# Kernel tuning notes

Hardware: AMD Instinct MI355X
Metric: run time of the kernel (lower is better)

Reference implementation:

```python
import jax, jax.numpy as jnp
import numpy as np

N_OBJ, N_REL = 2048, 32768
OBJ_DIM, POOL, H, E, C = 4096, 2048, 512, 200, 151
GEO = 128
IMG_W, IMG_H = 1024.0, 768.0
NUM_ITER = 3


def _lin(x, W, b):
    return x @ W.T + b


def _gru(x, h, Wih, Whh, bih, bhh):
    # torch.nn.GRUCell math; gates stacked (r, z, n)
    gi = x @ Wih.T + bih
    gh = h @ Whh.T + bhh
    i_r, i_z, i_n = jnp.split(gi, 3, axis=-1)
    h_r, h_z, h_n = jnp.split(gh, 3, axis=-1)
    r = jax.nn.sigmoid(i_r + h_r)
    z = jax.nn.sigmoid(i_z + h_z)
    n = jnp.tanh(i_n + r * h_n)
    return (1.0 - z) * n + z * h


def _box_info(boxes, norm=None):
    # [x1,y1,x2,y2,cx,cy,w,h]
    wh = boxes[:, 2:4] - boxes[:, 0:2] + 1.0
    ctr = boxes[:, 0:2] + 0.5 * wh
    info = jnp.concatenate([boxes, ctr, wh], axis=1)
    return info / norm if norm is not None else info


def _box_pair_info(b1, b2):
    # b1,b2: [R,8] normalized box infos -> [R,32]
    ub = jnp.stack([jnp.minimum(b1[:, 0], b2[:, 0]), jnp.minimum(b1[:, 1], b2[:, 1]),
                    jnp.maximum(b1[:, 2], b2[:, 2]), jnp.maximum(b1[:, 3], b2[:, 3])], axis=1)
    ib = jnp.stack([jnp.maximum(b1[:, 0], b2[:, 0]), jnp.maximum(b1[:, 1], b2[:, 1]),
                    jnp.minimum(b1[:, 2], b2[:, 2]), jnp.minimum(b1[:, 3], b2[:, 3])], axis=1)
    inter = _box_info(ib)
    bad = (ib[:, 2] < ib[:, 0]) | (ib[:, 3] < ib[:, 1])
    inter = jnp.where(bad[:, None], 0.0, inter)
    return jnp.concatenate([b1, b2, _box_info(ub), inter], axis=1)


def _encode_box_info(boxes):
    # motifs 9-d geometry encoding
    wh = boxes[:, 2:4] - boxes[:, 0:2] + 1.0
    xy = boxes[:, 0:2] + 0.5 * wh
    w, h = wh[:, 0:1], wh[:, 1:2]
    x, y = xy[:, 0:1], xy[:, 1:2]
    x1, y1, x2, y2 = boxes[:, 0:1], boxes[:, 1:2], boxes[:, 2:3], boxes[:, 3:4]
    return jnp.concatenate([w / IMG_W, h / IMG_H, x / IMG_W, y / IMG_H, x1 / IMG_W,
                            y1 / IMG_H, x2 / IMG_W, y2 / IMG_H, w * h / (IMG_W * IMG_H)], axis=1)


def _forward(inst_roi_feats, union_features, boxes, emb_dist_W, emb_label_W, up_W, up_b,
             pairup_W, pairup_b, pos1_W, pos1_b, bn_g, bn_b, bn_m, bn_v, pos2_W, pos2_b,
             spt1_W, spt1_b, spt2_W, spt2_b, pairfin_W, pairfin_b, objhid_W, objhid_b,
             objfin_W, objfin_b, objU_W, objU_b, edgeU_W, edgeU_b,
             egru_Wih, egru_Whh, egru_bih, egru_bhh, ngru_Wih, ngru_Whh, ngru_bih, ngru_bhh,
             svw_W, svw_b, ovw_W, ovw_b, obj_labels, sub_idx, obj_idx):
    # ---- PairwiseFeatureExtractor ----
    # pos_embed: fc(9,32) -> eval BatchNorm1d(32) -> fc(32,128) -> ReLU
    p = _lin(_encode_box_info(boxes), pos1_W, pos1_b)
    p = (p - bn_m) * bn_g / jnp.sqrt(bn_v + 1e-5) + bn_b
    pos_embed = jax.nn.relu(_lin(p, pos2_W, pos2_b))
    emb_dist = emb_dist_W[obj_labels]                       # predcls: embed GT labels
    aug = _lin(jnp.concatenate([inst_roi_feats, emb_dist, pos_embed], 1), objhid_W, objhid_b)
    augment = jnp.concatenate([emb_label_W[obj_labels], inst_roi_feats, aug], 1)  # [N,4808]
    # pairwise (edge) features: gather head/tail reps + spatial gating
    obox = _box_info(boxes, norm=max(IMG_W, IMG_H, 100.0))  # [N,8]
    fused = _lin(augment, pairup_W, pairup_b).reshape(-1, 2, H)
    pair = jnp.concatenate([fused[:, 0][sub_idx], fused[:, 1][obj_idx]], 1)  # [R,1024]
    geo = _box_pair_info(obox[sub_idx], obox[obj_idx])      # [R,32]
    spt = jax.nn.relu(_lin(jax.nn.relu(_lin(geo, spt1_W, spt1_b)), spt2_W, spt2_b))
    rel_feats = jax.nn.relu(_lin(pair * spt, pairfin_W, pairfin_b))
    rel_feats = rel_feats + _lin(union_features, up_W, up_b)  # 'fusion' + dim-up
    obj_feats = jax.nn.relu(_lin(augment, objfin_W, objfin_b))
    # ---- IMP iterative message passing ----
    obj_rep = _lin(obj_feats, objU_W, objU_b)
    rel_rep = jax.nn.relu(_lin(rel_feats, edgeU_W, edgeU_b))
    vert = _gru(obj_rep, jnp.zeros_like(obj_rep), ngru_Wih, ngru_Whh, ngru_bih, ngru_bhh)
    edge = _gru(rel_rep, jnp.zeros_like(rel_rep), egru_Wih, egru_Whh, egru_bih, egru_bhh)
    n = vert.shape[0]
    for _ in range(NUM_ITER):
        sv, ov = vert[sub_idx], vert[obj_idx]
        ws = jax.nn.sigmoid(_lin(jnp.concatenate([sv, edge], 1), svw_W, svw_b))  # [R,1]
        wo = jax.nn.sigmoid(_lin(jnp.concatenate([ov, edge], 1), ovw_W, ovw_b))
        new_edge = _gru(ws * sv + wo * ov, edge, egru_Wih, egru_Whh, egru_bih, egru_bhh)
        # sub2rel @ (ws*edge) + obj2rel @ (wo*edge) == segment sums over pair indices
        ctx = jax.ops.segment_sum(ws * edge, sub_idx, n) + jax.ops.segment_sum(wo * edge, obj_idx, n)
        vert = _gru(ctx, vert, ngru_Wih, ngru_Whh, ngru_bih, ngru_bhh)
        edge = new_edge
    return vert, edge


def setup_inputs() -> dict:
    keys = jax.random.split(jax.random.key(0), 64)
    ki = iter(keys)

    def nrm(shape, s=0.02):
        return (jax.random.normal(next(ki), shape) * s).astype(jnp.float32)

    kb = jax.random.split(next(ki), 4)
    x1 = jax.random.uniform(kb[0], (N_OBJ,)) * (IMG_W - 200.0)
    y1 = jax.random.uniform(kb[1], (N_OBJ,)) * (IMG_H - 150.0)
    x2 = x1 + 1.0 + jax.random.uniform(kb[2], (N_OBJ,)) * 199.0
    y2 = y1 + 1.0 + jax.random.uniform(kb[3], (N_OBJ,)) * 149.0
    boxes = jnp.stack([x1, y1, x2, y2], axis=1).astype(jnp.float32)

    inp = {
        'inst_roi_feats': nrm((N_OBJ, OBJ_DIM), 1.0),
        'union_features': nrm((N_REL, OBJ_DIM), 1.0),
        'boxes': boxes,
        'emb_dist_W': nrm((C, E)), 'emb_label_W': nrm((C, E)),
        'up_W': nrm((POOL, OBJ_DIM)), 'up_b': jnp.zeros((POOL,), jnp.float32),
        'pairup_W': nrm((2 * H, H + OBJ_DIM + E)), 'pairup_b': jnp.zeros((2 * H,), jnp.float32),
        'pos1_W': nrm((32, 9)), 'pos1_b': jnp.zeros((32,), jnp.float32),
        'bn_g': jnp.ones((32,), jnp.float32), 'bn_b': jnp.zeros((32,), jnp.float32),
        'bn_m': nrm((32,)), 'bn_v': jnp.ones((32,), jnp.float32),
        'pos2_W': nrm((GEO, 32)), 'pos2_b': jnp.zeros((GEO,), jnp.float32),
        'spt1_W': nrm((H, 32)), 'spt1_b': jnp.zeros((H,), jnp.float32),
        'spt2_W': nrm((2 * H, H)), 'spt2_b': jnp.zeros((2 * H,), jnp.float32),
        'pairfin_W': nrm((POOL, 2 * H)), 'pairfin_b': jnp.zeros((POOL,), jnp.float32),
        'objhid_W': nrm((H, OBJ_DIM + E + GEO)), 'objhid_b': jnp.zeros((H,), jnp.float32),
        'objfin_W': nrm((POOL, H + OBJ_DIM + E)), 'objfin_b': jnp.zeros((POOL,), jnp.float32),
        'objU_W': nrm((H, POOL)), 'objU_b': jnp.zeros((H,), jnp.float32),
        'edgeU_W': nrm((H, POOL)), 'edgeU_b': jnp.zeros((H,), jnp.float32),
        'egru_Wih': nrm((3 * H, H)), 'egru_Whh': nrm((3 * H, H)),
        'egru_bih': jnp.zeros((3 * H,), jnp.float32), 'egru_bhh': jnp.zeros((3 * H,), jnp.float32),
        'ngru_Wih': nrm((3 * H, H)), 'ngru_Whh': nrm((3 * H, H)),
        'ngru_bih': jnp.zeros((3 * H,), jnp.float32), 'ngru_bhh': jnp.zeros((3 * H,), jnp.float32),
        'svw_W': nrm((1, 2 * H)), 'svw_b': jnp.zeros((1,), jnp.float32),
        'ovw_W': nrm((1, 2 * H)), 'ovw_b': jnp.zeros((1,), jnp.float32),
        'obj_labels': jax.random.randint(next(ki), (N_OBJ,), 0, C),
        'sub_idx': jax.random.randint(next(ki), (N_REL,), 0, N_OBJ),
        'obj_idx': jax.random.randint(next(ki), (N_REL,), 0, N_OBJ),
    }
    return inp


def reference(inst_roi_feats, union_features, boxes, emb_dist_W, emb_label_W, up_W, up_b,
              pairup_W, pairup_b, pos1_W, pos1_b, bn_g, bn_b, bn_m, bn_v, pos2_W, pos2_b,
              spt1_W, spt1_b, spt2_W, spt2_b, pairfin_W, pairfin_b, objhid_W, objhid_b,
              objfin_W, objfin_b, objU_W, objU_b, edgeU_W, edgeU_b,
              egru_Wih, egru_Whh, egru_bih, egru_bhh, ngru_Wih, ngru_Whh, ngru_bih, ngru_bhh,
              svw_W, svw_b, ovw_W, ovw_b, obj_labels, sub_idx, obj_idx):
    return _forward(inst_roi_feats, union_features, boxes, emb_dist_W, emb_label_W, up_W, up_b,
                    pairup_W, pairup_b, pos1_W, pos1_b, bn_g, bn_b, bn_m, bn_v, pos2_W, pos2_b,
                    spt1_W, spt1_b, spt2_W, spt2_b, pairfin_W, pairfin_b, objhid_W, objhid_b,
                    objfin_W, objfin_b, objU_W, objU_b, edgeU_W, edgeU_b,
                    egru_Wih, egru_Whh, egru_bih, egru_bhh, ngru_Wih, ngru_Whh, ngru_bih, ngru_bhh,
                    svw_W, svw_b, ovw_W, ovw_b, obj_labels, sub_idx, obj_idx)
```

## Files before the change

kernel.cpp:

```cpp
#include <hip/hip_runtime.h>
#include <stdint.h>

#define NOBJ 2048
#define NREL 32768

typedef __attribute__((ext_vector_type(8))) short short8;
typedef __attribute__((ext_vector_type(4))) float f32x4;
typedef __attribute__((ext_vector_type(4))) unsigned short ushort4v;

__device__ __forceinline__ unsigned short f2bs(float x){
  unsigned u = __float_as_uint(x);
  unsigned v = u + 0x7fffu + ((u >> 16) & 1u);
  return (unsigned short)(v >> 16);
}
__device__ __forceinline__ float b2f(unsigned short u){
  return __uint_as_float(((unsigned)u) << 16);
}
__device__ __forceinline__ float sigf(float x){ return 1.0f / (1.0f + expf(-x)); }

__device__ __forceinline__ void gload16(const unsigned short* g, unsigned short* l) {
  __builtin_amdgcn_global_load_lds(
      (const __attribute__((address_space(1))) unsigned int*)(uintptr_t)g,
      (__attribute__((address_space(3))) unsigned int*)(uintptr_t)l,
      16, 0, 0);
}

template<int RMODE, bool ACCUM, bool OUTB, bool PRODF, bool AF32>
__global__ __launch_bounds__(256, 2)
void gemm_bt(const void* __restrict__ Ap, const unsigned short* __restrict__ B,
             const float* __restrict__ bias, const float* __restrict__ Cin,
             void* __restrict__ Cp, int M, int N, int K, int lda, int ldc,
             const unsigned short* __restrict__ fusedp,
             const int* __restrict__ subp, const int* __restrict__ objp)
{
  __shared__ __align__(16) unsigned short As[128 * 64];
  __shared__ __align__(16) unsigned short Bs[128 * 64];
  const int t = threadIdx.x;
  const int lane = t & 63;
  const int w = t >> 6;
  const int nwg = gridDim.x;
  const int q8 = nwg >> 3, r8 = nwg & 7;
  const int xcd = blockIdx.x & 7, bidx = blockIdx.x >> 3;
  const int wgid = (xcd < r8 ? xcd * (q8 + 1) : r8 * (q8 + 1) + (xcd - r8) * q8) + bidx;
  const int ntile = N >> 7;
  const int bm = wgid / ntile;
  const int bn = wgid - bm * ntile;
  const int m0 = bm << 7, n0 = bn << 7;
  const int wm = (w & 1) << 6, wn = (w >> 1) << 6;
  const int lrow = lane & 15, kg = lane >> 4;
  const int rx = lrow & 7;

  const int srow8 = lane >> 3;
  const int sslot = ((lane & 7) ^ srow8) << 3;
  const unsigned short* Bg = B + (long)(n0 + w * 8 + srow8) * K + sslot;
  const long ldb32 = (long)32 * K;

  const unsigned short* Ag = nullptr;
  const float* afp = nullptr;
  long lda32 = 0;
  int ar0 = 0;
  unsigned short* abase = nullptr;
  if constexpr (AF32) {
    ar0 = t >> 4;
    const int ac4 = t & 15;
    afp = (const float*)Ap + (long)(m0 + ar0) * lda + (ac4 << 2);
    abase = As + ((((ac4 >> 1) ^ (ar0 & 7)) << 3) + ((ac4 & 1) << 2));
  } else {
    Ag = (const unsigned short*)Ap + (long)(m0 + w * 8 + srow8) * lda + sslot;
    lda32 = (long)32 * lda;
  }

  f32x4 acc[4][4] = {};

  for (int k0 = 0; k0 < K; k0 += 64) {
#pragma unroll
    for (int q = 0; q < 4; q++)
      gload16(Bg + q * ldb32 + k0, Bs + (q * 32 + w * 8) * 64);
    if constexpr (AF32) {
      const float* ap = afp + k0;
#pragma unroll
      for (int j = 0; j < 8; j++) {
        f32x4 v = *(const f32x4*)(ap + (long)j * 16 * lda);
        ushort4v o;
        o[0] = f2bs(v[0]); o[1] = f2bs(v[1]); o[2] = f2bs(v[2]); o[3] = f2bs(v[3]);
        *(ushort4v*)(abase + (ar0 + j * 16) * 64) = o;
      }
    } else {
#pragma unroll
      for (int q = 0; q < 4; q++)
        gload16(Ag + q * lda32 + k0, As + (q * 32 + w * 8) * 64);
    }
    __syncthreads();
    short8 afr[4][2], bfr[4][2];
#pragma unroll
    for (int i = 0; i < 4; i++) {
      const int ra = wm + i * 16 + lrow;
#pragma unroll
      for (int ks = 0; ks < 2; ks++)
        afr[i][ks] = *(const short8*)(As + ra * 64 + (((ks * 4 + kg) ^ rx) << 3));
    }
#pragma unroll
    for (int j = 0; j < 4; j++) {
      const int rb = wn + j * 16 + lrow;
#pragma unroll
      for (int ks = 0; ks < 2; ks++)
        bfr[j][ks] = *(const short8*)(Bs + rb * 64 + (((ks * 4 + kg) ^ rx) << 3));
    }
#pragma unroll
    for (int i = 0; i < 4; i++)
#pragma unroll
      for (int j = 0; j < 4; j++)
#pragma unroll
        for (int ks = 0; ks < 2; ks++)
          acc[i][j] = __builtin_amdgcn_mfma_f32_16x16x32_bf16(afr[i][ks], bfr[j][ks], acc[i][j], 0, 0, 0);
    __syncthreads();
  }

  float* Cf = (float*)Cp;
  unsigned short* Cb = (unsigned short*)Cp;
#pragma unroll
  for (int i = 0; i < 4; i++) {
#pragma unroll
    for (int j = 0; j < 4; j++) {
      const int col = n0 + wn + j * 16 + lrow;
      const float bv = bias[col];
#pragma unroll
      for (int q = 0; q < 4; q++) {
        const long row = m0 + wm + i * 16 + kg * 4 + q;
        float v = acc[i][j][q] + bv;
        if constexpr (RMODE == 1) v = fmaxf(v, 0.0f);
        if constexpr (PRODF) {
          int gr = (col < 512) ? subp[row] : objp[row];
          v *= b2f(fusedp[(long)gr * 1024 + col]);
        }
        if constexpr (ACCUM) v += Cin[row * (long)N + col];
        if constexpr (RMODE == 2) v = fmaxf(v, 0.0f);
        if constexpr (OUTB) Cb[row * (long)ldc + col] = f2bs(v);
        else Cf[row * (long)ldc + col] = v;
      }
    }
  }
}


__global__ void cvt_pad4(const float* __restrict__ src, unsigned short* __restrict__ dst,
                         int rows, int K0, int Kp)
{
  const int kp4 = Kp >> 2;
  const long total = (long)rows * kp4;
  for (long i = blockIdx.x * (long)blockDim.x + threadIdx.x; i < total; i += (long)gridDim.x * blockDim.x) {
    int r = (int)(i / kp4), k = (int)(i - (long)r * kp4) << 2;
    ushort4v o;
    if (k < K0) {
      f32x4 v = *(const f32x4*)(src + (long)r * K0 + k);
      o[0] = f2bs(v[0]); o[1] = f2bs(v[1]); o[2] = f2bs(v[2]); o[3] = f2bs(v[3]);
    } else {
      o[0] = 0; o[1] = 0; o[2] = 0; o[3] = 0;
    }
    *(ushort4v*)(dst + (long)r * Kp + k) = o;
  }
}

__global__ void cvt4(const float* __restrict__ src, unsigned short* __restrict__ dst, long n4)
{
  for (long i = blockIdx.x * (long)blockDim.x + threadIdx.x; i < n4; i += (long)gridDim.x * blockDim.x) {
    f32x4 v = ((const f32x4*)src)[i];
    ushort4v o;
    o[0] = f2bs(v[0]); o[1] = f2bs(v[1]); o[2] = f2bs(v[2]); o[3] = f2bs(v[3]);
    ((ushort4v*)dst)[i] = o;
  }
}

__global__ void transpose_cvt(const float* __restrict__ src, unsigned short* __restrict__ dst,
                              int R, int C)
{
  __shared__ float tile[32][33];
  int c0 = blockIdx.x * 32, r0 = blockIdx.y * 32;
  for (int i = threadIdx.y; i < 32; i += 8)
    tile[i][threadIdx.x] = src[(long)(r0 + i) * C + c0 + threadIdx.x];
  __syncthreads();
  for (int i = threadIdx.y; i < 32; i += 8)
    dst[(long)(c0 + i) * R + r0 + threadIdx.x] = f2bs(tile[threadIdx.x][i]);
}

__global__ void comp_bias(const float* __restrict__ edgeU_W, const float* __restrict__ up_b,
                          const float* __restrict__ edgeU_b, float* __restrict__ b_comp)
{
  int j = (int)((blockIdx.x * (long)blockDim.x + threadIdx.x) >> 6);
  int l = threadIdx.x & 63;
  if (j >= 512) return;
  float s = 0.0f;
  for (int k = l; k < 2048; k += 64) s += edgeU_W[(long)j * 2048 + k] * up_b[k];
#pragma unroll
  for (int off = 32; off > 0; off >>= 1) s += __shfl_xor(s, off);
  if (l == 0) b_comp[j] = s + edgeU_b[j];
}

__global__ void bias_cat(const float* __restrict__ bhh, float* __restrict__ out)
{
  int j = blockIdx.x * blockDim.x + threadIdx.x;
  if (j < 3072) out[j] = (j < 1536) ? 0.0f : bhh[j - 1536];
}

__global__ void obox_k(const float* __restrict__ boxes, float* __restrict__ obox)
{
  int i = blockIdx.x * blockDim.x + threadIdx.x;
  if (i >= NOBJ) return;
  float x1 = boxes[i*4], y1 = boxes[i*4+1], x2 = boxes[i*4+2], y2 = boxes[i*4+3];
  float wdt = x2 - x1 + 1.0f, hgt = y2 - y1 + 1.0f;
  float cx = x1 + 0.5f * wdt, cy = y1 + 0.5f * hgt;
  const float inv = 1.0f / 1024.0f;
  float* o = obox + i * 8;
  o[0]=x1*inv; o[1]=y1*inv; o[2]=x2*inv; o[3]=y2*inv;
  o[4]=cx*inv; o[5]=cy*inv; o[6]=wdt*inv; o[7]=hgt*inv;
}

__global__ void posembed_k(const float* __restrict__ boxes,
                           const float* __restrict__ w1, const float* __restrict__ b1,
                           const float* __restrict__ g, const float* __restrict__ bb,
                           const float* __restrict__ mm, const float* __restrict__ vv,
                           const float* __restrict__ w2, const float* __restrict__ b2,
                           float* __restrict__ out)
{
  int o = blockIdx.x, t = threadIdx.x;
  __shared__ float e[9];
  __shared__ float p[32];
  if (t == 0) {
    float x1 = boxes[o*4], y1 = boxes[o*4+1], x2 = boxes[o*4+2], y2 = boxes[o*4+3];
    float wdt = x2 - x1 + 1.0f, hgt = y2 - y1 + 1.0f;
    float cx = x1 + 0.5f * wdt, cy = y1 + 0.5f * hgt;
    e[0]=wdt/1024.0f; e[1]=hgt/768.0f; e[2]=cx/1024.0f; e[3]=cy/768.0f;
    e[4]=x1/1024.0f;  e[5]=y1/768.0f;  e[6]=x2/1024.0f; e[7]=y2/768.0f;
    e[8]=wdt*hgt/(1024.0f*768.0f);
  }
  __syncthreads();
  if (t < 32) {
    float s = b1[t];
#pragma unroll
    for (int j = 0; j < 9; j++) s += w1[t*9+j] * e[j];
    s = (s - mm[t]) * g[t] / sqrtf(vv[t] + 1e-5f) + bb[t];
    p[t] = s;
  }
  __syncthreads();
  float s = b2[t];
#pragma unroll
  for (int j = 0; j < 32; j++) s += w2[t*32+j] * p[j];
  out[o*128 + t] = fmaxf(s, 0.0f);
}

__device__ __forceinline__ void pack8_store(unsigned short* dst, f32x4 a, f32x4 b)
{
  ushort4v o0, o1;
  o0[0]=f2bs(a[0]); o0[1]=f2bs(a[1]); o0[2]=f2bs(a[2]); o0[3]=f2bs(a[3]);
  o1[0]=f2bs(b[0]); o1[1]=f2bs(b[1]); o1[2]=f2bs(b[2]); o1[3]=f2bs(b[3]);
  *(ushort4v*)dst = o0;
  *(ushort4v*)(dst + 4) = o1;
}

__global__ void build_x1(const float* __restrict__ inst, const float* __restrict__ embd,
                         const int* __restrict__ labels, const float* __restrict__ pose,
                         unsigned short* __restrict__ X1b)
{
  const long total = (long)NOBJ * 560;
  for (long i = blockIdx.x * (long)blockDim.x + threadIdx.x; i < total; i += (long)gridDim.x * blockDim.x) {
    int r = (int)(i / 560), c = ((int)(i - (long)r * 560)) << 3;
    unsigned short* dst = X1b + (long)r * 4480 + c;
    const float* src;
    if (c < 4096)      src = inst + (long)r * 4096 + c;
    else if (c < 4296) src = embd + (long)labels[r] * 200 + (c - 4096);
    else if (c < 4424) src = pose + r * 128 + (c - 4296);
    else { ushort4v z = {0,0,0,0}; *(ushort4v*)dst = z; *(ushort4v*)(dst+4) = z; continue; }
    pack8_store(dst, *(const f32x4*)src, *((const f32x4*)src + 1));
  }
}

__global__ void build_aug(const float* __restrict__ embl, const int* __restrict__ labels,
                          const float* __restrict__ inst, unsigned short* __restrict__ augb)
{
  const long total = (long)NOBJ * 608;
  for (long i = blockIdx.x * (long)blockDim.x + threadIdx.x; i < total; i += (long)gridDim.x * blockDim.x) {
    int r = (int)(i / 608), c = ((int)(i - (long)r * 608)) << 3;
    if (c >= 4296 && c < 4808) continue;
    unsigned short* dst = augb + (long)r * 4864 + c;
    const float* src;
    if (c < 200)       src = embl + (long)labels[r] * 200 + c;
    else if (c < 4296) src = inst + (long)r * 4096 + (c - 200);
    else { ushort4v z = {0,0,0,0}; *(ushort4v*)dst = z; *(ushort4v*)(dst+4) = z; continue; }
    pack8_store(dst, *(const f32x4*)src, *((const f32x4*)src + 1));
  }
}

__global__ void build_geo(const float* __restrict__ obox, const int* __restrict__ sub,
                          const int* __restrict__ obj, unsigned short* __restrict__ geob)
{
  int r = blockIdx.x * blockDim.x + threadIdx.x;
  if (r >= NREL) return;
  const float* b1 = obox + sub[r] * 8;
  const float* b2 = obox + obj[r] * 8;
  float o[32];
#pragma unroll
  for (int j = 0; j < 8; j++) { o[j] = b1[j]; o[8+j] = b2[j]; }
  float ux1 = fminf(b1[0], b2[0]), uy1 = fminf(b1[1], b2[1]);
  float ux2 = fmaxf(b1[2], b2[2]), uy2 = fmaxf(b1[3], b2[3]);
  float uw = ux2 - ux1 + 1.0f, uh = uy2 - uy1 + 1.0f;
  o[16]=ux1; o[17]=uy1; o[18]=ux2; o[19]=uy2;
  o[20]=ux1+0.5f*uw; o[21]=uy1+0.5f*uh; o[22]=uw; o[23]=uh;
  float ix1 = fmaxf(b1[0], b2[0]), iy1 = fmaxf(b1[1], b2[1]);
  float ix2 = fminf(b1[2], b2[2]), iy2 = fminf(b1[3], b2[3]);
  bool bad = (ix2 < ix1) || (iy2 < iy1);
  float iw = ix2 - ix1 + 1.0f, ih = iy2 - iy1 + 1.0f;
  if (bad) {
#pragma unroll
    for (int j = 24; j < 32; j++) o[j] = 0.0f;
  } else {
    o[24]=ix1; o[25]=iy1; o[26]=ix2; o[27]=iy2;
    o[28]=ix1+0.5f*iw; o[29]=iy1+0.5f*ih; o[30]=iw; o[31]=ih;
  }
  unsigned short* gp = geob + (long)r * 64;
#pragma unroll
  for (int j = 0; j < 32; j++) gp[j] = f2bs(o[j]);
#pragma unroll
  for (int j = 32; j < 64; j++) gp[j] = 0;
}

__global__ void gru_init_v(const unsigned short* __restrict__ gi, const float* __restrict__ bhh,
                           float* __restrict__ h, unsigned short* __restrict__ hb, int n)
{
  const long total = (long)n * 64;
  for (long i = blockIdx.x * (long)blockDim.x + threadIdx.x; i < total; i += (long)gridDim.x * blockDim.x) {
    int r = (int)(i >> 6), c = ((int)(i & 63)) << 3;
    const unsigned short* gr = gi + (long)r * 1536;
    short8 vr = *(const short8*)(gr + c);
    short8 vz = *(const short8*)(gr + 512 + c);
    short8 vn = *(const short8*)(gr + 1024 + c);
    float hv[8];
#pragma unroll
    for (int k = 0; k < 8; k++) {
      float rr = sigf(b2f((unsigned short)vr[k]) + bhh[c + k]);
      float z  = sigf(b2f((unsigned short)vz[k]) + bhh[512 + c + k]);
      float nn = tanhf(b2f((unsigned short)vn[k]) + rr * bhh[1024 + c + k]);
      hv[k] = (1.0f - z) * nn;
    }
    float* hp = h + (long)r * 512 + c;
    *(f32x4*)hp = *(f32x4*)hv;
    *(f32x4*)(hp + 4) = *(f32x4*)(hv + 4);
    pack8_store(hb + (long)r * 512 + c, *(f32x4*)hv, *(f32x4*)(hv + 4));
  }
}

__global__ void gru_init_e(const unsigned short* __restrict__ gi, const float* __restrict__ bhh,
                           unsigned short* __restrict__ hb, int n)
{
  const long total = (long)n * 64;
  for (long i = blockIdx.x * (long)blockDim.x + threadIdx.x; i < total; i += (long)gridDim.x * blockDim.x) {
    int r = (int)(i >> 6), c = ((int)(i & 63)) << 3;
    const unsigned short* gr = gi + (long)r * 1536;
    short8 vr = *(const short8*)(gr + c);
    short8 vz = *(const short8*)(gr + 512 + c);
    short8 vn = *(const short8*)(gr + 1024 + c);
    float hv[8];
#pragma unroll
    for (int k = 0; k < 8; k++) {
      float rr = sigf(b2f((unsigned short)vr[k]) + bhh[c + k]);
      float z  = sigf(b2f((unsigned short)vz[k]) + bhh[512 + c + k]);
      float nn = tanhf(b2f((unsigned short)vn[k]) + rr * bhh[1024 + c + k]);
      hv[k] = (1.0f - z) * nn;
    }
    pack8_store(hb + (long)r * 512 + c, *(f32x4*)hv, *(f32x4*)(hv + 4));
  }
}

__global__ void gru_step_v(const unsigned short* __restrict__ gi, const unsigned short* __restrict__ gh,
                           int ghs, const float* __restrict__ hin, float* __restrict__ hout,
                           unsigned short* __restrict__ hb, int n)
{
  const long total = (long)n * 64;
  for (long i = blockIdx.x * (long)blockDim.x + threadIdx.x; i < total; i += (long)gridDim.x * blockDim.x) {
    int r = (int)(i >> 6), c = ((int)(i & 63)) << 3;
    const unsigned short* gr = gi + (long)r * 1536;
    const unsigned short* hr = gh + (long)r * ghs;
    short8 ir = *(const short8*)(gr + c);
    short8 iz = *(const short8*)(gr + 512 + c);
    short8 in_ = *(const short8*)(gr + 1024 + c);
    short8 hrr = *(const short8*)(hr + c);
    short8 hz = *(const short8*)(hr + 512 + c);
    short8 hn = *(const short8*)(hr + 1024 + c);
    const float* hi = hin + (long)r * 512 + c;
    f32x4 h0 = *(const f32x4*)hi;
    f32x4 h1 = *(const f32x4*)(hi + 4);
    float hv[8];
#pragma unroll
    for (int k = 0; k < 8; k++) {
      float rr = sigf(b2f((unsigned short)ir[k]) + b2f((unsigned short)hrr[k]));
      float z  = sigf(b2f((unsigned short)iz[k]) + b2f((unsigned short)hz[k]));
      float nn = tanhf(b2f((unsigned short)in_[k]) + rr * b2f((unsigned short)hn[k]));
      float old = (k < 4) ? h0[k] : h1[k - 4];
      hv[k] = (1.0f - z) * nn + z * old;
    }
    float* hp = hout + (long)r * 512 + c;
    *(f32x4*)hp = *(f32x4*)hv;
    *(f32x4*)(hp + 4) = *(f32x4*)(hv + 4);
    pack8_store(hb + (long)r * 512 + c, *(f32x4*)hv, *(f32x4*)(hv + 4));
  }
}

__global__ __launch_bounds__(256)
void gru_step_e2(const unsigned short* __restrict__ GH, const unsigned short* __restrict__ VG,
                 const float* __restrict__ ws_arr_in, const float* __restrict__ wo_arr_in,
                 float* __restrict__ ws_arr_out, float* __restrict__ wo_arr_out,
                 const int* __restrict__ sub, const int* __restrict__ obj,
                 const float* __restrict__ bih,
                 unsigned short* __restrict__ edgeb, float* __restrict__ fout,
                 const unsigned short* __restrict__ vertb,
                 const float* __restrict__ svwW, const float* __restrict__ svwb,
                 const float* __restrict__ ovwW, const float* __restrict__ ovwb,
                 int compute_w, int n)
{
  long gid = blockIdx.x * 256L + threadIdx.x;
  int r = (int)(gid >> 6);
  int l = (int)(gid & 63);
  if (r >= n) return;
  const int c = l << 3;
  int s = sub[r], o = obj[r];
  float ws = ws_arr_in[r], wo = wo_arr_in[r];
  const unsigned short* gh = GH + (long)r * 1536;
  const unsigned short* vs = VG + (long)s * 3072;
  const unsigned short* vo = VG + (long)o * 3072;
  short8 ghr = *(const short8*)(gh + c);
  short8 ghz = *(const short8*)(gh + 512 + c);
  short8 ghn = *(const short8*)(gh + 1024 + c);
  short8 vsr = *(const short8*)(vs + c);
  short8 vsz = *(const short8*)(vs + 512 + c);
  short8 vsn = *(const short8*)(vs + 1024 + c);
  short8 vor_ = *(const short8*)(vo + c);
  short8 voz = *(const short8*)(vo + 512 + c);
  short8 von = *(const short8*)(vo + 1024 + c);
  short8 hold = *(const short8*)(edgeb + (long)r * 512 + c);
  float hv[8];
#pragma unroll
  for (int k = 0; k < 8; k++) {
    float gir = ws * b2f((unsigned short)vsr[k]) + wo * b2f((unsigned short)vor_[k]) + bih[c + k];
    float giz = ws * b2f((unsigned short)vsz[k]) + wo * b2f((unsigned short)voz[k]) + bih[512 + c + k];
    float gin = ws * b2f((unsigned short)vsn[k]) + wo * b2f((unsigned short)von[k]) + bih[1024 + c + k];
    float rr = sigf(gir + b2f((unsigned short)ghr[k]));
    float z  = sigf(giz + b2f((unsigned short)ghz[k]));
    float nn = tanhf(gin + rr * b2f((unsigned short)ghn[k]));
    hv[k] = (1.0f - z) * nn + z * b2f((unsigned short)hold[k]);
  }
  pack8_store(edgeb + (long)r * 512 + c, *(f32x4*)hv, *(f32x4*)(hv + 4));
  if (fout) {
    float* fp = fout + (long)r * 512 + c;
    *(f32x4*)fp = *(f32x4*)hv;
    *(f32x4*)(fp + 4) = *(f32x4*)(hv + 4);
  }
  if (compute_w) {
    short8 svv = *(const short8*)(vertb + (long)s * 512 + c);
    short8 ovv = *(const short8*)(vertb + (long)o * 512 + c);
    float as = 0.0f, ao = 0.0f;
#pragma unroll
    for (int k = 0; k < 8; k++) {
      float e = hv[k];
      as += svwW[c + k] * b2f((unsigned short)svv[k]) + svwW[512 + c + k] * e;
      ao += ovwW[c + k] * b2f((unsigned short)ovv[k]) + ovwW[512 + c + k] * e;
    }
#pragma unroll
    for (int off = 32; off > 0; off >>= 1) {
      as += __shfl_xor(as, off);
      ao += __shfl_xor(ao, off);
    }
    if (l == 0) {
      ws_arr_out[r] = sigf(as + svwb[0]);
      wo_arr_out[r] = sigf(ao + ovwb[0]);
    }
  }
}

__global__ __launch_bounds__(256)
void edge_weights(const unsigned short* __restrict__ vertb, const unsigned short* __restrict__ edgeb,
                  const int* __restrict__ sub, const int* __restrict__ obj,
                  const float* __restrict__ svwW, const float* __restrict__ svwb,
                  const float* __restrict__ ovwW, const float* __restrict__ ovwb,
                  float* __restrict__ ws_arr, float* __restrict__ wo_arr)
{
  long gid = blockIdx.x * 256L + threadIdx.x;
  int r = (int)(gid >> 6);
  int l = (int)(gid & 63);
  if (r >= NREL) return;
  int s = sub[r], o = obj[r];
  const unsigned short* sv = vertb + (long)s * 512;
  const unsigned short* ov = vertb + (long)o * 512;
  const unsigned short* e  = edgeb + (long)r * 512;
  float as = 0.0f, ao = 0.0f;
#pragma unroll
  for (int k = 0; k < 8; k++) {
    int c = l + k * 64;
    float svv = b2f(sv[c]), ovv = b2f(ov[c]), ev = b2f(e[c]);
    as += svwW[c] * svv + svwW[512 + c] * ev;
    ao += ovwW[c] * ovv + ovwW[512 + c] * ev;
  }
#pragma unroll
  for (int off = 32; off > 0; off >>= 1) {
    as += __shfl_xor(as, off);
    ao += __shfl_xor(ao, off);
  }
  if (l == 0) {
    ws_arr[r] = sigf(as + svwb[0]);
    wo_arr[r] = sigf(ao + ovwb[0]);
  }
}


__global__ void csr_count(const int* __restrict__ sub, const int* __restrict__ obj,
                          int* __restrict__ cnt)
{
  int r = blockIdx.x * blockDim.x + threadIdx.x;
  if (r >= NREL) return;
  atomicAdd(&cnt[sub[r]], 1);
  atomicAdd(&cnt[obj[r]], 1);
}

__global__ __launch_bounds__(1024)
void csr_scan(const int* __restrict__ cnt, int* __restrict__ off)
{
  __shared__ int a[1024], b[1024];
  int t = threadIdx.x;
  int c0 = cnt[2*t], c1 = cnt[2*t+1];
  a[t] = c0 + c1;
  __syncthreads();
  int* src = a; int* dst = b;
  for (int s = 1; s < 1024; s <<= 1) {
    int v = src[t];
    if (t >= s) v += src[t - s];
    dst[t] = v;
    __syncthreads();
    int* tmp = src; src = dst; dst = tmp;
  }
  int incl = src[t];
  int excl = incl - (c0 + c1);
  off[2*t] = excl;
  off[2*t+1] = excl + c0;
  if (t == 1023) off[2048] = incl;
}

__global__ void csr_fill(const int* __restrict__ sub, const int* __restrict__ obj,
                         const int* __restrict__ off, int* __restrict__ rcur,
                         int* __restrict__ lists)
{
  int r = blockIdx.x * blockDim.x + threadIdx.x;
  if (r >= NREL) return;
  int s = sub[r];
  int p = atomicAdd(&rcur[s], 1);
  lists[off[s] + p] = (r << 1);
  int o = obj[r];
  int q = atomicAdd(&rcur[o], 1);
  lists[off[o] + q] = (r << 1) | 1;
}

__global__ __launch_bounds__(128)
void ctx_gather(const unsigned short* __restrict__ edgeb, const float* __restrict__ ws,
                const float* __restrict__ wo, const int* __restrict__ off,
                const int* __restrict__ lists, unsigned short* __restrict__ ctxb)
{
  __shared__ float part[512];
  int o = blockIdx.x;
  int l = threadIdx.x & 63;
  int w = threadIdx.x >> 6;
  int i0 = off[o], i1 = off[o + 1];
  float acc[8] = {0.f,0.f,0.f,0.f,0.f,0.f,0.f,0.f};
  for (int i = i0 + w; i < i1; i += 2) {
    int e = lists[i];
    int r = e >> 1;
    float sc = (e & 1) ? wo[r] : ws[r];
    short8 row = *(const short8*)(edgeb + (long)r * 512 + l * 8);
#pragma unroll
    for (int k = 0; k < 8; k++) acc[k] += sc * b2f((unsigned short)row[k]);
  }
  if (w == 1) {
    *(f32x4*)&part[l*8]     = *(f32x4*)&acc[0];
    *(f32x4*)&part[l*8 + 4] = *(f32x4*)&acc[4];
  }
  __syncthreads();
  if (w == 0) {
#pragma unroll
    for (int k = 0; k < 8; k++) acc[k] += part[l*8 + k];
    pack8_store(ctxb + (long)o * 512 + l * 8, *(f32x4*)&acc[0], *(f32x4*)&acc[4]);
  }
}


static inline int nblk(long total) {
  long b = (total + 255) / 256;
  return (int)(b > 16384 ? 16384 : b);
}

#define GEMM(RM, AC, OB, PF, grid, Aa, Bb, bb, Ci, Cc, Mm, Nn, Kk, ldA, ldC, fp, sp, op) \
  gemm_bt<RM, AC, OB, PF, false><<<grid, 256, 0, stream>>>(Aa, Bb, bb, Ci, Cc, Mm, Nn, Kk, ldA, ldC, fp, sp, op)
#define GEMMF(RM, AC, OB, grid, Aa, Bb, bb, Ci, Cc, Mm, Nn, Kk, ldA, ldC) \
  gemm_bt<RM, AC, OB, false, true><<<grid, 256, 0, stream>>>(Aa, Bb, bb, Ci, Cc, Mm, Nn, Kk, ldA, ldC, nullptr, nullptr, nullptr)

extern "C" void kernel_launch(void* const* d_in, const int* in_sizes, int n_in,
                              void* d_out, int out_size, void* d_ws, size_t ws_size,
                              hipStream_t stream)
{
  const float* inst     = (const float*)d_in[0];
  const float* unionf   = (const float*)d_in[1];
  const float* boxes    = (const float*)d_in[2];
  const float* embd_W   = (const float*)d_in[3];
  const float* embl_W   = (const float*)d_in[4];
  const float* up_W     = (const float*)d_in[5];
  const float* up_b     = (const float*)d_in[6];
  const float* pairup_W = (const float*)d_in[7];
  const float* pairup_b = (const float*)d_in[8];
  const float* pos1_W   = (const float*)d_in[9];
  const float* pos1_b   = (const float*)d_in[10];
  const float* bn_g     = (const float*)d_in[11];
  const float* bn_b     = (const float*)d_in[12];
  const float* bn_m     = (const float*)d_in[13];
  const float* bn_v     = (const float*)d_in[14];
  const float* pos2_W   = (const float*)d_in[15];
  const float* pos2_b   = (const float*)d_in[16];
  const float* spt1_W   = (const float*)d_in[17];
  const float* spt1_b   = (const float*)d_in[18];
  const float* spt2_W   = (const float*)d_in[19];
  const float* spt2_b   = (const float*)d_in[20];
  const float* pairfin_W= (const float*)d_in[21];
  const float* pairfin_b= (const float*)d_in[22];
  const float* objhid_W = (const float*)d_in[23];
  const float* objhid_b = (const float*)d_in[24];
  const float* objfin_W = (const float*)d_in[25];
  const float* objfin_b = (const float*)d_in[26];
  const float* objU_W   = (const float*)d_in[27];
  const float* objU_b   = (const float*)d_in[28];
  const float* edgeU_W  = (const float*)d_in[29];
  const float* edgeU_b  = (const float*)d_in[30];
  const float* egru_Wih = (const float*)d_in[31];
  const float* egru_Whh = (const float*)d_in[32];
  const float* egru_bih = (const float*)d_in[33];
  const float* egru_bhh = (const float*)d_in[34];
  const float* ngru_Wih = (const float*)d_in[35];
  const float* ngru_Whh = (const float*)d_in[36];
  const float* ngru_bih = (const float*)d_in[37];
  const float* ngru_bhh = (const float*)d_in[38];
  const float* svw_W    = (const float*)d_in[39];
  const float* svw_b    = (const float*)d_in[40];
  const float* ovw_W    = (const float*)d_in[41];
  const float* ovw_b    = (const float*)d_in[42];
  const int*   labels   = (const int*)d_in[43];
  const int*   sub      = (const int*)d_in[44];
  const int*   obj      = (const int*)d_in[45];
  (void)in_sizes; (void)n_in; (void)out_size; (void)ws_size;

  char* base = (char*)d_ws;
  size_t off = 0;
  auto alloc = [&](size_t bytes) -> void* {
    void* p = base + off;
    off += (bytes + 255) & ~(size_t)255;
    return p;
  };

  unsigned short* objhid_Wb  = (unsigned short*)alloc(512L  * 4480 * 2);
  unsigned short* pairup_Wb  = (unsigned short*)alloc(1024L * 4864 * 2);
  unsigned short* objfin_Wb  = (unsigned short*)alloc(2048L * 4864 * 2);
  unsigned short* up_Wtb     = (unsigned short*)alloc(4096L * 2048 * 2);
  unsigned short* pairfin_Wb = (unsigned short*)alloc(2048L * 1024 * 2);
  unsigned short* spt1_Wb    = (unsigned short*)alloc(512L  * 64   * 2);
  unsigned short* spt2_Wb    = (unsigned short*)alloc(1024L * 512  * 2);
  unsigned short* objU_Wb    = (unsigned short*)alloc(512L  * 2048 * 2);
  unsigned short* edgeU_Wb   = (unsigned short*)alloc(512L  * 2048 * 2);
  unsigned short* egru_Wihb  = (unsigned short*)alloc(1536L * 512  * 2);
  unsigned short* egru_Whhb  = (unsigned short*)alloc(1536L * 512  * 2);
  unsigned short* ngru_Wihb  = (unsigned short*)alloc(1536L * 512  * 2);
  unsigned short* vg_Wb      = (unsigned short*)alloc(3072L * 512  * 2);
  unsigned short* W_compb    = (unsigned short*)alloc(512L  * 4096 * 2);
  float*          b_comp     = (float*)alloc(512L * 4);
  float*          zbias      = (float*)alloc(4096L * 4);
  float*          vgbias     = (float*)alloc(3072L * 4);

  float*          obox      = (float*)alloc(NOBJ * 8L * 4);
  float*          pose      = (float*)alloc(NOBJ * 128L * 4);
  unsigned short* obj_featsb= (unsigned short*)alloc((long)NOBJ * 2048 * 2);
  unsigned short* obj_repb  = (unsigned short*)alloc((long)NOBJ * 512 * 2);
  unsigned short* giv       = (unsigned short*)alloc((long)NOBJ * 1536 * 2);
  unsigned short* VGb       = (unsigned short*)alloc((long)NOBJ * 3072 * 2);
  float*          vert      = (float*)alloc((long)NOBJ * 512 * 4);
  unsigned short* vertb     = (unsigned short*)alloc((long)NOBJ * 512 * 2);
  unsigned short* ctxb      = (unsigned short*)alloc((long)NOBJ * 512 * 2);
  unsigned short* geob      = (unsigned short*)alloc((long)NREL * 64 * 2);
  unsigned short* edgeb     = (unsigned short*)alloc((long)NREL * 512 * 2);
  float*          ws_arr    = (float*)alloc((long)NREL * 4);
  float*          wo_arr    = (float*)alloc((long)NREL * 4);

  int* cnt   = (int*)alloc(NOBJ * 4);
  int* coff  = (int*)alloc((NOBJ + 1) * 4);
  int* rcur  = (int*)alloc(NOBJ * 4);
  int* lists = (int*)alloc(2L * NREL * 4);

  char* regA = (char*)alloc((long)NREL * 512 * 4);
  unsigned short* X1b = (unsigned short*)regA;
  float*          T1  = (float*)regA;
  char* regB = (char*)alloc((long)NOBJ * 4864 * 2 > (long)NREL * 512 * 2
                            ? (long)NOBJ * 4864 * 2 : (long)NREL * 512 * 2);
  unsigned short* augb     = (unsigned short*)regB;
  unsigned short* rel_repb = (unsigned short*)regB;
  unsigned short* fusedb = (unsigned short*)alloc((long)NOBJ * 1024 * 2);
  unsigned short* spt1b  = (unsigned short*)alloc((long)NREL * 512 * 2);
  char* big1 = (char*)alloc((long)NREL * 1536 * 4);
  unsigned short* G1    = (unsigned short*)big1;
  unsigned short* prodb = (unsigned short*)(big1 + (long)NREL * 1024 * 4);
  unsigned short* gi_e  = (unsigned short*)big1;
  unsigned short* GHb   = (unsigned short*)big1;

  float* d_out_vert = (float*)d_out;
  float* d_out_edge = (float*)d_out + (long)NOBJ * 512;

  cvt_pad4<<<nblk(512L*4480/4),  256, 0, stream>>>(objhid_W,  objhid_Wb,  512,  4424, 4480);
  cvt_pad4<<<nblk(1024L*4864/4), 256, 0, stream>>>(pairup_W,  pairup_Wb,  1024, 4808, 4864);
  cvt_pad4<<<nblk(2048L*4864/4), 256, 0, stream>>>(objfin_W,  objfin_Wb,  2048, 4808, 4864);
  cvt_pad4<<<nblk(512L*64/4),    256, 0, stream>>>(spt1_W,    spt1_Wb,    512,  32,   64);
  cvt4<<<nblk(2048L*1024/4), 256, 0, stream>>>(pairfin_W, pairfin_Wb, 2048L*1024/4);
  cvt4<<<nblk(1024L*512/4),  256, 0, stream>>>(spt2_W,    spt2_Wb,    1024L*512/4);
  cvt4<<<nblk(512L*2048/4),  256, 0, stream>>>(objU_W,    objU_Wb,    512L*2048/4);
  cvt4<<<nblk(512L*2048/4),  256, 0, stream>>>(edgeU_W,   edgeU_Wb,   512L*2048/4);
  cvt4<<<nblk(1536L*512/4),  256, 0, stream>>>(egru_Wih,  egru_Wihb,  1536L*512/4);
  cvt4<<<nblk(1536L*512/4),  256, 0, stream>>>(egru_Whh,  egru_Whhb,  1536L*512/4);
  cvt4<<<nblk(1536L*512/4),  256, 0, stream>>>(ngru_Wih,  ngru_Wihb,  1536L*512/4);
  cvt4<<<nblk(1536L*512/4),  256, 0, stream>>>(egru_Wih,  vg_Wb,               1536L*512/4);
  cvt4<<<nblk(1536L*512/4),  256, 0, stream>>>(ngru_Whh,  vg_Wb + 1536L*512,   1536L*512/4);
  bias_cat<<<12, 256, 0, stream>>>(ngru_bhh, vgbias);
  transpose_cvt<<<dim3(4096/32, 2048/32), dim3(32, 8), 0, stream>>>(up_W, up_Wtb, 2048, 4096);
  hipMemsetAsync(zbias, 0, 4096L * 4, stream);
  comp_bias<<<128, 256, 0, stream>>>(edgeU_W, up_b, edgeU_b, b_comp);
  GEMM(0,false,true,false, dim3((512>>7)*(4096>>7)), edgeU_Wb, up_Wtb, zbias, nullptr, W_compb, 512, 4096, 2048, 2048, 4096, nullptr, nullptr, nullptr);

  hipMemsetAsync(cnt, 0, NOBJ * 4, stream);
  hipMemsetAsync(rcur, 0, NOBJ * 4, stream);
  csr_count<<<NREL/256, 256, 0, stream>>>(sub, obj, cnt);
  csr_scan<<<1, 1024, 0, stream>>>(cnt, coff);
  csr_fill<<<NREL/256, 256, 0, stream>>>(sub, obj, coff, rcur, lists);

  obox_k<<<(NOBJ + 255) / 256, 256, 0, stream>>>(boxes, obox);
  posembed_k<<<NOBJ, 128, 0, stream>>>(boxes, pos1_W, pos1_b, bn_g, bn_b, bn_m, bn_v,
                                       pos2_W, pos2_b, pose);
  build_x1<<<nblk((long)NOBJ*560), 256, 0, stream>>>(inst, embd_W, labels, pose, X1b);
  build_aug<<<nblk((long)NOBJ*608), 256, 0, stream>>>(embl_W, labels, inst, augb);
  GEMM(0,false,true ,false, dim3((NOBJ>>7)*(512>>7)),  X1b, objhid_Wb, objhid_b, nullptr, augb + 4296, NOBJ, 512, 4480, 4480, 4864, nullptr, nullptr, nullptr);
  GEMM(0,false,true ,false, dim3((NOBJ>>7)*(1024>>7)), augb, pairup_Wb, pairup_b, nullptr, fusedb, NOBJ, 1024, 4864, 4864, 1024, nullptr, nullptr, nullptr);
  GEMM(1,false,true ,false, dim3((NOBJ>>7)*(2048>>7)), augb, objfin_Wb, objfin_b, nullptr, obj_featsb, NOBJ, 2048, 4864, 4864, 2048, nullptr, nullptr, nullptr);
  GEMM(0,false,true ,false, dim3((NOBJ>>7)*(512>>7)),  obj_featsb, objU_Wb, objU_b, nullptr, obj_repb, NOBJ, 512, 2048, 2048, 512, nullptr, nullptr, nullptr);
  GEMM(0,false,true ,false, dim3((NOBJ>>7)*(1536>>7)), obj_repb, ngru_Wihb, ngru_bih, nullptr, giv, NOBJ, 1536, 512, 512, 1536, nullptr, nullptr, nullptr);
  gru_init_v<<<nblk((long)NOBJ*64), 256, 0, stream>>>(giv, ngru_bhh, vert, vertb, NOBJ);

  build_geo<<<(NREL + 255) / 256, 256, 0, stream>>>(obox, sub, obj, geob);
  GEMM(1,false,true ,false, dim3((NREL>>7)*(512>>7)),  geob, spt1_Wb, spt1_b, nullptr, spt1b, NREL, 512, 64, 64, 512, nullptr, nullptr, nullptr);
  GEMM(1,false,true ,true , dim3((NREL>>7)*(1024>>7)), spt1b, spt2_Wb, spt2_b, nullptr, prodb, NREL, 1024, 512, 512, 1024, fusedb, sub, obj);
  GEMM(1,false,true ,false, dim3((NREL>>7)*(2048>>7)), prodb, pairfin_Wb, pairfin_b, nullptr, G1, NREL, 2048, 1024, 1024, 2048, nullptr, nullptr, nullptr);
  GEMMF(0,false,false, dim3((NREL>>7)*(512>>7)), unionf, W_compb, b_comp, nullptr, T1, NREL, 512, 4096, 4096, 512);
  GEMM(2,true ,true ,false, dim3((NREL>>7)*(512>>7)),  G1, edgeU_Wb, zbias, T1, rel_repb, NREL, 512, 2048, 2048, 512, nullptr, nullptr, nullptr);
  GEMM(0,false,true ,false, dim3((NREL>>7)*(1536>>7)), rel_repb, egru_Wihb, egru_bih, nullptr, gi_e, NREL, 1536, 512, 512, 1536, nullptr, nullptr, nullptr);
  gru_init_e<<<nblk((long)NREL*64), 256, 0, stream>>>(gi_e, egru_bhh, edgeb, NREL);

  edge_weights<<<NREL*64/256, 256, 0, stream>>>(vertb, edgeb, sub, obj,
                                                svw_W, svw_b, ovw_W, ovw_b, ws_arr, wo_arr);

  for (int it = 0; it < 3; it++) {
    const bool last = (it == 2);
    ctx_gather<<<NOBJ, 128, 0, stream>>>(edgeb, ws_arr, wo_arr, coff, lists, ctxb);
    GEMM(0,false,true,false, dim3((NOBJ>>7)*(3072>>7)), vertb, vg_Wb, vgbias, nullptr, VGb, NOBJ, 3072, 512, 512, 3072, nullptr, nullptr, nullptr);
    GEMM(0,false,true,false, dim3((NREL>>7)*(1536>>7)), edgeb, egru_Whhb, egru_bhh, nullptr, GHb, NREL, 1536, 512, 512, 1536, nullptr, nullptr, nullptr);
    GEMM(0,false,true,false, dim3((NOBJ>>7)*(1536>>7)), ctxb, ngru_Wihb, ngru_bih, nullptr, giv, NOBJ, 1536, 512, 512, 1536, nullptr, nullptr, nullptr);
    gru_step_v<<<nblk((long)NOBJ*64), 256, 0, stream>>>(giv, VGb + 1536, 3072, vert,
                                                        last ? d_out_vert : vert, vertb, NOBJ);
    gru_step_e2<<<NREL*64/256, 256, 0, stream>>>(GHb, VGb, ws_arr, wo_arr, ws_arr, wo_arr,
                                                 sub, obj, egru_bih, edgeb,
                                                 last ? d_out_edge : nullptr, vertb,
                                                 svw_W, svw_b, ovw_W, ovw_b,
                                                 last ? 0 : 1, NREL);
  }
}
```

Baseline: 1.820 ms.

## Use 64x64-tile GEMM for small-M object GEMMs and batch weight conversions

Adds a 64x64-tile bf16 MFMA GEMM kernel with XCD-aware block remapping and uses it for the object-side GEMMs (M=2048 or 512). These previously launched too few 128x128 tiles to fill the GPU. The nine separate fp32-to-bf16 weight conversion launches are also merged into one multi-segment kernel to save launch overhead. The smaller tiles give more workgroups but less data reuse per tile and a single-buffered K loop.

```diff
diff --git a/kernel.cpp b/kernel.cpp
--- a/kernel.cpp
+++ b/kernel.cpp
@@ -142,6 +142,84 @@
   }
 }
 
+template<int RMODE>
+__global__ __launch_bounds__(256, 2)
+void gemm64(const unsigned short* __restrict__ A, const unsigned short* __restrict__ B,
+            const float* __restrict__ bias, unsigned short* __restrict__ C,
+            int M, int N, int K, int lda, int ldc)
+{
+  __shared__ __align__(16) unsigned short As[64 * 64];
+  __shared__ __align__(16) unsigned short Bs[64 * 64];
+  const int t = threadIdx.x;
+  const int lane = t & 63;
+  const int w = t >> 6;
+  const int nwg = gridDim.x;
+  const int q8 = nwg >> 3, r8 = nwg & 7;
+  const int xcd = blockIdx.x & 7, bidx = blockIdx.x >> 3;
+  const int wgid = (xcd < r8 ? xcd * (q8 + 1) : r8 * (q8 + 1) + (xcd - r8) * q8) + bidx;
+  const int ntile = N >> 6;
+  const int bm = wgid / ntile, bn = wgid - bm * ntile;
+  const int m0 = bm << 6, n0 = bn << 6;
+  const int wm = (w & 1) << 5, wn = (w >> 1) << 5;
+  const int lrow = lane & 15, kg = lane >> 4;
+  const int rx = lrow & 7;
+
+  const int srow8 = lane >> 3;
+  const int sslot = ((lane & 7) ^ srow8) << 3;
+  const unsigned short* Ag = A + (long)(m0 + w * 16 + srow8) * lda + sslot;
+  const unsigned short* Bg = B + (long)(n0 + w * 16 + srow8) * K + sslot;
+  const long lda8 = 8L * lda, ldb8 = 8L * K;
+
+  f32x4 acc[2][2] = {};
+
+  for (int k0 = 0; k0 < K; k0 += 64) {
+    gload16(Ag + k0,        As + (w * 16) * 64);
+    gload16(Ag + lda8 + k0, As + (w * 16 + 8) * 64);
+    gload16(Bg + k0,        Bs + (w * 16) * 64);
+    gload16(Bg + ldb8 + k0, Bs + (w * 16 + 8) * 64);
+    __syncthreads();
+    short8 afr[2][2], bfr[2][2];
+#pragma unroll
+    for (int i = 0; i < 2; i++) {
+      const int ra = wm + i * 16 + lrow;
+#pragma unroll
+      for (int ks = 0; ks < 2; ks++)
+        afr[i][ks] = *(const short8*)(As + ra * 64 + (((ks * 4 + kg) ^ rx) << 3));
+    }
+#pragma unroll
+    for (int j = 0; j < 2; j++) {
+      const int rb = wn + j * 16 + lrow;
+#pragma unroll
+      for (int ks = 0; ks < 2; ks++)
+        bfr[j][ks] = *(const short8*)(Bs + rb * 64 + (((ks * 4 + kg) ^ rx) << 3));
+    }
+#pragma unroll
+    for (int i = 0; i < 2; i++)
+#pragma unroll
+      for (int j = 0; j < 2; j++)
+#pragma unroll
+        for (int ks = 0; ks < 2; ks++)
+          acc[i][j] = __builtin_amdgcn_mfma_f32_16x16x32_bf16(afr[i][ks], bfr[j][ks], acc[i][j], 0, 0, 0);
+    __syncthreads();
+  }
+
+#pragma unroll
+  for (int i = 0; i < 2; i++) {
+#pragma unroll
+    for (int j = 0; j < 2; j++) {
+      const int col = n0 + wn + j * 16 + lrow;
+      const float bv = bias[col];
+#pragma unroll
+      for (int q = 0; q < 4; q++) {
+        const long row = m0 + wm + i * 16 + kg * 4 + q;
+        float v = acc[i][j][q] + bv;
+        if constexpr (RMODE == 1) v = fmaxf(v, 0.0f);
+        C[row * (long)ldc + col] = f2bs(v);
+      }
+    }
+  }
+}
+
 
 __global__ void cvt_pad4(const float* __restrict__ src, unsigned short* __restrict__ dst,
                          int rows, int K0, int Kp)
@@ -161,13 +239,24 @@
   }
 }
 
-__global__ void cvt4(const float* __restrict__ src, unsigned short* __restrict__ dst, long n4)
-{
-  for (long i = blockIdx.x * (long)blockDim.x + threadIdx.x; i < n4; i += (long)gridDim.x * blockDim.x) {
-    f32x4 v = ((const f32x4*)src)[i];
-    ushort4v o;
-    o[0] = f2bs(v[0]); o[1] = f2bs(v[1]); o[2] = f2bs(v[2]); o[3] = f2bs(v[3]);
-    ((ushort4v*)dst)[i] = o;
+struct CvtSeg { const float* src; unsigned short* dst; long base; long n4; };
+struct Cvt9 { CvtSeg s[9]; long total; };
+
+__global__ void cvt4_multi(Cvt9 cfg)
+{
+  for (long i = blockIdx.x * (long)blockDim.x + threadIdx.x; i < cfg.total;
+       i += (long)gridDim.x * blockDim.x) {
+#pragma unroll
+    for (int k = 0; k < 9; k++) {
+      if (i >= cfg.s[k].base && i < cfg.s[k].base + cfg.s[k].n4) {
+        long j = i - cfg.s[k].base;
+        f32x4 v = ((const f32x4*)cfg.s[k].src)[j];
+        ushort4v o;
+        o[0] = f2bs(v[0]); o[1] = f2bs(v[1]); o[2] = f2bs(v[2]); o[3] = f2bs(v[3]);
+        ((ushort4v*)cfg.s[k].dst)[j] = o;
+        break;
+      }
+    }
   }
 }
 
@@ -597,6 +686,8 @@
   gemm_bt<RM, AC, OB, PF, false><<<grid, 256, 0, stream>>>(Aa, Bb, bb, Ci, Cc, Mm, Nn, Kk, ldA, ldC, fp, sp, op)
 #define GEMMF(RM, AC, OB, grid, Aa, Bb, bb, Ci, Cc, Mm, Nn, Kk, ldA, ldC) \
   gemm_bt<RM, AC, OB, false, true><<<grid, 256, 0, stream>>>(Aa, Bb, bb, Ci, Cc, Mm, Nn, Kk, ldA, ldC, nullptr, nullptr, nullptr)
+#define G64(RM, Aa, Bb, bb, Cc, Mm, Nn, Kk, ldA, ldC) \
+  gemm64<RM><<<dim3(((Mm) >> 6) * ((Nn) >> 6)), 256, 0, stream>>>(Aa, Bb, bb, Cc, Mm, Nn, Kk, ldA, ldC)
 
 extern "C" void kernel_launch(void* const* d_in, const int* in_sizes, int n_in,
                               void* d_out, int out_size, void* d_ws, size_t ws_size,
@@ -717,20 +808,29 @@
   cvt_pad4<<<nblk(1024L*4864/4), 256, 0, stream>>>(pairup_W,  pairup_Wb,  1024, 4808, 4864);
   cvt_pad4<<<nblk(2048L*4864/4), 256, 0, stream>>>(objfin_W,  objfin_Wb,  2048, 4808, 4864);
   cvt_pad4<<<nblk(512L*64/4),    256, 0, stream>>>(spt1_W,    spt1_Wb,    512,  32,   64);
-  cvt4<<<nblk(2048L*1024/4), 256, 0, stream>>>(pairfin_W, pairfin_Wb, 2048L*1024/4);
-  cvt4<<<nblk(1024L*512/4),  256, 0, stream>>>(spt2_W,    spt2_Wb,    1024L*512/4);
-  cvt4<<<nblk(512L*2048/4),  256, 0, stream>>>(objU_W,    objU_Wb,    512L*2048/4);
-  cvt4<<<nblk(512L*2048/4),  256, 0, stream>>>(edgeU_W,   edgeU_Wb,   512L*2048/4);
-  cvt4<<<nblk(1536L*512/4),  256, 0, stream>>>(egru_Wih,  egru_Wihb,  1536L*512/4);
-  cvt4<<<nblk(1536L*512/4),  256, 0, stream>>>(egru_Whh,  egru_Whhb,  1536L*512/4);
-  cvt4<<<nblk(1536L*512/4),  256, 0, stream>>>(ngru_Wih,  ngru_Wihb,  1536L*512/4);
-  cvt4<<<nblk(1536L*512/4),  256, 0, stream>>>(egru_Wih,  vg_Wb,               1536L*512/4);
-  cvt4<<<nblk(1536L*512/4),  256, 0, stream>>>(ngru_Whh,  vg_Wb + 1536L*512,   1536L*512/4);
+  {
+    Cvt9 cfg;
+    long b = 0;
+    auto seg = [&](int k, const float* s, unsigned short* d, long n4) {
+      cfg.s[k].src = s; cfg.s[k].dst = d; cfg.s[k].base = b; cfg.s[k].n4 = n4; b += n4;
+    };
+    seg(0, pairfin_W, pairfin_Wb, 2048L*1024/4);
+    seg(1, spt2_W,    spt2_Wb,    1024L*512/4);
+    seg(2, objU_W,    objU_Wb,    512L*2048/4);
+    seg(3, edgeU_W,   edgeU_Wb,   512L*2048/4);
+    seg(4, egru_Wih,  egru_Wihb,  1536L*512/4);
+    seg(5, egru_Whh,  egru_Whhb,  1536L*512/4);
+    seg(6, ngru_Wih,  ngru_Wihb,  1536L*512/4);
+    seg(7, egru_Wih,  vg_Wb,              1536L*512/4);
+    seg(8, ngru_Whh,  vg_Wb + 1536L*512,  1536L*512/4);
+    cfg.total = b;
+    cvt4_multi<<<nblk(b), 256, 0, stream>>>(cfg);
+  }
   bias_cat<<<12, 256, 0, stream>>>(ngru_bhh, vgbias);
   transpose_cvt<<<dim3(4096/32, 2048/32), dim3(32, 8), 0, stream>>>(up_W, up_Wtb, 2048, 4096);
   hipMemsetAsync(zbias, 0, 4096L * 4, stream);
   comp_bias<<<128, 256, 0, stream>>>(edgeU_W, up_b, edgeU_b, b_comp);
-  GEMM(0,false,true,false, dim3((512>>7)*(4096>>7)), edgeU_Wb, up_Wtb, zbias, nullptr, W_compb, 512, 4096, 2048, 2048, 4096, nullptr, nullptr, nullptr);
+  G64(0, edgeU_Wb, up_Wtb, zbias, W_compb, 512, 4096, 2048, 2048, 4096);
 
   hipMemsetAsync(cnt, 0, NOBJ * 4, stream);
   hipMemsetAsync(rcur, 0, NOBJ * 4, stream);
@@ -743,11 +843,11 @@
                                        pos2_W, pos2_b, pose);
   build_x1<<<nblk((long)NOBJ*560), 256, 0, stream>>>(inst, embd_W, labels, pose, X1b);
   build_aug<<<nblk((long)NOBJ*608), 256, 0, stream>>>(embl_W, labels, inst, augb);
-  GEMM(0,false,true ,false, dim3((NOBJ>>7)*(512>>7)),  X1b, objhid_Wb, objhid_b, nullptr, augb + 4296, NOBJ, 512, 4480, 4480, 4864, nullptr, nullptr, nullptr);
-  GEMM(0,false,true ,false, dim3((NOBJ>>7)*(1024>>7)), augb, pairup_Wb, pairup_b, nullptr, fusedb, NOBJ, 1024, 4864, 4864, 1024, nullptr, nullptr, nullptr);
-  GEMM(1,false,true ,false, dim3((NOBJ>>7)*(2048>>7)), augb, objfin_Wb, objfin_b, nullptr, obj_featsb, NOBJ, 2048, 4864, 4864, 2048, nullptr, nullptr, nullptr);
-  GEMM(0,false,true ,false, dim3((NOBJ>>7)*(512>>7)),  obj_featsb, objU_Wb, objU_b, nullptr, obj_repb, NOBJ, 512, 2048, 2048, 512, nullptr, nullptr, nullptr);
-  GEMM(0,false,true ,false, dim3((NOBJ>>7)*(1536>>7)), obj_repb, ngru_Wihb, ngru_bih, nullptr, giv, NOBJ, 1536, 512, 512, 1536, nullptr, nullptr, nullptr);
+  G64(0, X1b, objhid_Wb, objhid_b, augb + 4296, NOBJ, 512, 4480, 4480, 4864);
+  G64(0, augb, pairup_Wb, pairup_b, fusedb, NOBJ, 1024, 4864, 4864, 1024);
+  G64(1, augb, objfin_Wb, objfin_b, obj_featsb, NOBJ, 2048, 4864, 4864, 2048);
+  G64(0, obj_featsb, objU_Wb, objU_b, obj_repb, NOBJ, 512, 2048, 2048, 512);
+  G64(0, obj_repb, ngru_Wihb, ngru_bih, giv, NOBJ, 1536, 512, 512, 1536);
   gru_init_v<<<nblk((long)NOBJ*64), 256, 0, stream>>>(giv, ngru_bhh, vert, vertb, NOBJ);
 
   build_geo<<<(NREL + 255) / 256, 256, 0, stream>>>(obox, sub, obj, geob);
@@ -765,9 +865,9 @@
   for (int it = 0; it < 3; it++) {
     const bool last = (it == 2);
     ctx_gather<<<NOBJ, 128, 0, stream>>>(edgeb, ws_arr, wo_arr, coff, lists, ctxb);
-    GEMM(0,false,true,false, dim3((NOBJ>>7)*(3072>>7)), vertb, vg_Wb, vgbias, nullptr, VGb, NOBJ, 3072, 512, 512, 3072, nullptr, nullptr, nullptr);
+    G64(0, vertb, vg_Wb, vgbias, VGb, NOBJ, 3072, 512, 512, 3072);
     GEMM(0,false,true,false, dim3((NREL>>7)*(1536>>7)), edgeb, egru_Whhb, egru_bhh, nullptr, GHb, NREL, 1536, 512, 512, 1536, nullptr, nullptr, nullptr);
-    GEMM(0,false,true,false, dim3((NOBJ>>7)*(1536>>7)), ctxb, ngru_Wihb, ngru_bih, nullptr, giv, NOBJ, 1536, 512, 512, 1536, nullptr, nullptr, nullptr);
+    G64(0, ctxb, ngru_Wihb, ngru_bih, giv, NOBJ, 1536, 512, 512, 1536);
     gru_step_v<<<nblk((long)NOBJ*64), 256, 0, stream>>>(giv, VGb + 1536, 3072, vert,
                                                         last ? d_out_vert : vert, vertb, NOBJ);
     gru_step_e2<<<NREL*64/256, 256, 0, stream>>>(GHb, VGb, ws_arr, wo_arr, ws_arr, wo_arr,
```

Result: faster. 1.695 ms (-6.9%).
